# Kernel tuning notes

Measured on AMD Instinct MI355X. Metric: run time of the kernel, lower is better.

## Reference

```python
import jax, jax.numpy as jnp
import numpy as np

B, NQ, NK, DIM, H = 2, 2048, 4096, 256, 8
HD = DIM // H  # head dim = 32


def setup_inputs() -> dict:
    key = jax.random.key(0)
    ks = jax.random.split(key, 8)
    s = 0.02  # init scale for weights
    return {
        "xq": jax.random.normal(ks[0], (B, NQ, DIM), jnp.float32),
        "xk": jax.random.normal(ks[1], (B, NK, DIM), jnp.float32),
        "xv": jax.random.normal(ks[2], (B, NK, DIM), jnp.float32),
        # torch nn.Linear weights: shape (out, in), y = x @ W.T + b
        "wq": jax.random.normal(ks[3], (DIM, DIM), jnp.float32) * s,
        "wk": jax.random.normal(ks[4], (DIM, DIM), jnp.float32) * s,
        "wv": jax.random.normal(ks[5], (DIM, DIM), jnp.float32) * s,
        "wp": jax.random.normal(ks[6], (DIM, DIM), jnp.float32) * s,
        "bp": jnp.zeros((DIM,), jnp.float32),
    }


def reference(xq, xk, xv, wq, wk, wv, wp, bp):
    scale = HD ** (-0.5)
    Bq, Nq, C = xq.shape
    Nk = xk.shape[1]
    # project and split heads: [B, H, N, HD]
    q = jnp.einsum('bnc,dc->bnd', xq, wq).reshape(Bq, Nq, H, HD).transpose(0, 2, 1, 3)
    k = jnp.einsum('bnc,dc->bnd', xk, wk).reshape(Bq, Nk, H, HD).transpose(0, 2, 1, 3)
    v = jnp.einsum('bnc,dc->bnd', xv, wv).reshape(Bq, Nk, H, HD).transpose(0, 2, 1, 3)
    # pre-softmax scores [B, H, Nq, Nk]
    attn = jnp.einsum('bhqd,bhkd->bhqk', q, k) * scale
    attn_save = attn.sum(axis=1) / H  # head-mean of pre-softmax scores
    p = jax.nn.softmax(attn, axis=-1)
    x = jnp.einsum('bhqk,bhkd->bhqd', p, v).transpose(0, 2, 1, 3).reshape(Bq, Nq, C)
    x = jnp.einsum('bnc,dc->bnd', x, wp) + bp
    return x, attn_save
```

## Files before the change

### kernel.cpp

```cpp
#include <hip/hip_runtime.h>

typedef unsigned int u32;
typedef unsigned short u16;
typedef short bf16x8 __attribute__((ext_vector_type(8)));
typedef float f32x4 __attribute__((ext_vector_type(4)));
typedef int i32x4 __attribute__((ext_vector_type(4)));
typedef __bf16 bf16x2 __attribute__((ext_vector_type(2)));
typedef float f32x2 __attribute__((ext_vector_type(2)));

#define KSPLIT 4

__device__ __forceinline__ u32 pack2bf(float a, float b) {
    u32 ua = __float_as_uint(a), ub = __float_as_uint(b);
    ua = (ua + 0x7fffu + ((ua >> 16) & 1u)) >> 16;
    ub = (ub + 0x7fffu + ((ub >> 16) & 1u)) >> 16;
    return (ua & 0xffffu) | (ub << 16);
}
__device__ __forceinline__ u16 bf1(float a) {
    u32 ua = __float_as_uint(a);
    return (u16)((ua + 0x7fffu + ((ua >> 16) & 1u)) >> 16);
}
__device__ __forceinline__ u32 b2(float a, float b) {
    f32x2 f; f[0] = a; f[1] = b;
    bf16x2 h = __builtin_convertvector(f, bf16x2);
    return __builtin_bit_cast(u32, h);
}

__global__ __launch_bounds__(256) void cvt_w4(const float* __restrict__ wq,
                                              const float* __restrict__ wk,
                                              const float* __restrict__ wv,
                                              const float* __restrict__ wp,
                                              u16* __restrict__ dst) {
    int i = blockIdx.x * 256 + threadIdx.x;
    int which = i >> 14;
    int j = i & 16383;
    const float* s = which == 0 ? wq : which == 1 ? wk : which == 2 ? wv : wp;
    float4 a = ((const float4*)s)[j];
    uint2 v;
    v.x = pack2bf(a.x, a.y);
    v.y = pack2bf(a.z, a.w);
    ((uint2*)(dst + which * 65536))[j] = v;
}

__global__ __launch_bounds__(256) void proj_all(const float* __restrict__ xq,
                                                const float* __restrict__ xk,
                                                const float* __restrict__ xv,
                                                const u16* __restrict__ W4,
                                                u16* __restrict__ Qb,
                                                u16* __restrict__ K2,
                                                u16* __restrict__ V2,
                                                float qalpha) {
    int bx = blockIdx.x;
    int mode = bx < 64 ? 0 : (bx < 192 ? 1 : 2);
    int xb = mode == 0 ? bx : (mode == 1 ? bx - 64 : bx - 192);
    const float* X = mode == 0 ? xq : mode == 1 ? xk : xv;
    const u16* Wb = W4 + mode * 65536;

    __shared__ u16 xs[64 * 256];
    int t = threadIdx.x;
    int m0 = xb * 64;
#pragma unroll
    for (int i = 0; i < 8; i++) {
        int c16 = t + 256 * i;
        int row = c16 >> 5, col16 = c16 & 31;
        const float4* src = (const float4*)(X + (size_t)(m0 + row) * 256 + col16 * 8);
        float4 a = src[0], b2v = src[1];
        uint4 v;
        v.x = pack2bf(a.x, a.y); v.y = pack2bf(a.z, a.w);
        v.z = pack2bf(b2v.x, b2v.y); v.w = pack2bf(b2v.z, b2v.w);
        int byteoff = row * 512 + ((col16 * 16) ^ ((row & 7) << 4));
        *(uint4*)((char*)xs + byteoff) = v;
    }
    __syncthreads();
    int lane = t & 63, w = t >> 6;
    int lq = lane & 15, g = lane >> 4;
    int rowA = w * 16 + lq;
    f32x4 acc[16];
    f32x4 z = {0.f, 0.f, 0.f, 0.f};
#pragma unroll
    for (int nt = 0; nt < 16; nt++) acc[nt] = z;
#pragma unroll
    for (int kk = 0; kk < 8; kk++) {
        bf16x8 aF = *(const bf16x8*)((const char*)xs + rowA * 512 +
                                     ((kk * 64 + g * 16) ^ ((rowA & 7) << 4)));
#pragma unroll
        for (int nt = 0; nt < 16; nt++) {
            bf16x8 bF = *(const bf16x8*)(Wb + (size_t)(nt * 16 + lq) * 256 + kk * 32 + g * 8);
            acc[nt] = __builtin_amdgcn_mfma_f32_16x16x32_bf16(aF, bF, acc[nt], 0, 0, 0);
        }
    }
    if (mode == 0) {
#pragma unroll
        for (int nt = 0; nt < 16; nt++) {
            int col = nt * 16 + lq;
#pragma unroll
            for (int r = 0; r < 4; r++) {
                int m = m0 + w * 16 + g * 4 + r;
                Qb[(size_t)m * 256 + col] = bf1(acc[nt][r] * qalpha);
            }
        }
    } else if (mode == 1) {
        int m = m0 + w * 16 + g * 4;
        int b = m >> 12, n = m & 4095;
#pragma unroll
        for (int nt = 0; nt < 16; nt++) {
            int d = nt * 16 + lq;
            int h = d >> 5, d32 = d & 31;
            u16* p = K2 + ((size_t)(b * 8 + h) * 4096 + n) * 32 + d32;
#pragma unroll
            for (int r = 0; r < 4; r++) p[r * 32] = bf1(acc[nt][r]);
        }
    } else {
        int m = m0 + w * 16 + g * 4;
        int b = m >> 12, n = m & 4095;
        int s = n >> 5, rem = n & 31;
        int hp = rem >> 4, gp = (rem >> 2) & 3;
        int pklo = gp * 8 + hp * 4;
#pragma unroll
        for (int nt = 0; nt < 16; nt++) {
            int d = nt * 16 + lq;
            int h = d >> 5, d32 = d & 31;
            uint2 v;
            v.x = pack2bf(acc[nt][0], acc[nt][1]);
            v.y = pack2bf(acc[nt][2], acc[nt][3]);
            *(uint2*)(V2 + ((((size_t)(b * 8 + h) * 128 + s) * 32 + d32) * 32 + pklo)) = v;
        }
    }
}

__global__ __launch_bounds__(256) void save_gemm(const u16* __restrict__ Qb,
                                                 const u16* __restrict__ K2,
                                                 float* __restrict__ sv) {
    const float SAVE = 0.125f * 0.69314718055994530942f;
    int b = blockIdx.z;
    int m0 = blockIdx.y * 128, n0 = blockIdx.x * 128;
    int t = threadIdx.x, lane = t & 63, wv = t >> 6;
    int wr = wv >> 1, wc = wv & 1;
    int lq = lane & 15, g = lane >> 4;
    const u16* Q = Qb + (size_t)b * 2048 * 256;
    f32x4 acc[4][4];
    f32x4 z = {0.f, 0.f, 0.f, 0.f};
#pragma unroll
    for (int mt = 0; mt < 4; mt++)
#pragma unroll
        for (int nt = 0; nt < 4; nt++) acc[mt][nt] = z;
#pragma unroll
    for (int kk = 0; kk < 8; kk++) {
        bf16x8 aF[4], bF[4];
#pragma unroll
        for (int mt = 0; mt < 4; mt++)
            aF[mt] = *(const bf16x8*)(Q + (size_t)(m0 + wr * 64 + mt * 16 + lq) * 256 + kk * 32 + g * 8);
#pragma unroll
        for (int nt = 0; nt < 4; nt++)
            bF[nt] = *(const bf16x8*)(K2 + ((size_t)(b * 8 + kk) * 4096 + n0 + wc * 64 + nt * 16 + lq) * 32 + g * 8);
#pragma unroll
        for (int mt = 0; mt < 4; mt++)
#pragma unroll
            for (int nt = 0; nt < 4; nt++)
                acc[mt][nt] = __builtin_amdgcn_mfma_f32_16x16x32_bf16(aF[mt], bF[nt], acc[mt][nt], 0, 0, 0);
    }
#pragma unroll
    for (int mt = 0; mt < 4; mt++) {
#pragma unroll
        for (int nt = 0; nt < 4; nt++) {
            int col = n0 + wc * 64 + nt * 16 + lq;
#pragma unroll
            for (int r = 0; r < 4; r++) {
                int row = m0 + wr * 64 + mt * 16 + g * 4 + r;
                sv[((size_t)b * 2048 + row) * 4096 + col] = acc[mt][nt][r] * SAVE;
            }
        }
    }
}

__global__ __launch_bounds__(256, 4) void attn_part(const u16* __restrict__ Qb,
                                                    const u16* __restrict__ K2,
                                                    const u16* __restrict__ V2,
                                                    float* __restrict__ PO,
                                                    float* __restrict__ PL) {
    int b = blockIdx.z >> 2, part = blockIdx.z & 3, h = blockIdx.y;
    int bh = b * 8 + h;
    int t = threadIdx.x, lane = t & 63, w = t >> 6;
    int lq = lane & 15, g = lane >> 4;
    int qa = blockIdx.x * 128 + w * 32 + lq;
    const u16* Qrow = Qb + ((size_t)(b * 2048 + qa)) * 256 + h * 32 + g * 8;
    bf16x8 qFa = *(const bf16x8*)Qrow;
    bf16x8 qFb = *(const bf16x8*)(Qrow + 16 * 256);
    const u16* Kh = K2 + ((size_t)bh * 4096 + part * 1024 + lq) * 32 + g * 8;
    const u16* Vh = V2 + ((size_t)bh * 128 + part * 32) * 1024 + lq * 32 + g * 8;
    f32x4 z4 = {0.f, 0.f, 0.f, 0.f};
    f32x4 oa0 = z4, oa1 = z4, ob0 = z4, ob1 = z4, laa = z4, lab = z4;
    const short ONE = (short)0x3F80;
    bf16x8 onesF = {ONE, ONE, ONE, ONE, ONE, ONE, ONE, ONE};
    for (int it = 0; it < 16; ++it) {
        const u16* kp = Kh + it * 2048;
        bf16x8 kF0 = *(const bf16x8*)(kp);
        bf16x8 kF1 = *(const bf16x8*)(kp + 512);
        bf16x8 kF2 = *(const bf16x8*)(kp + 1024);
        bf16x8 kF3 = *(const bf16x8*)(kp + 1536);
        f32x4 sa[4], sb[4];
        sa[0] = __builtin_amdgcn_mfma_f32_16x16x32_bf16(kF0, qFa, z4, 0, 0, 0);
        sa[1] = __builtin_amdgcn_mfma_f32_16x16x32_bf16(kF1, qFa, z4, 0, 0, 0);
        sa[2] = __builtin_amdgcn_mfma_f32_16x16x32_bf16(kF2, qFa, z4, 0, 0, 0);
        sa[3] = __builtin_amdgcn_mfma_f32_16x16x32_bf16(kF3, qFa, z4, 0, 0, 0);
        sb[0] = __builtin_amdgcn_mfma_f32_16x16x32_bf16(kF0, qFb, z4, 0, 0, 0);
        sb[1] = __builtin_amdgcn_mfma_f32_16x16x32_bf16(kF1, qFb, z4, 0, 0, 0);
        sb[2] = __builtin_amdgcn_mfma_f32_16x16x32_bf16(kF2, qFb, z4, 0, 0, 0);
        sb[3] = __builtin_amdgcn_mfma_f32_16x16x32_bf16(kF3, qFb, z4, 0, 0, 0);
        u32 ua[8], ub[8];
#pragma unroll
        for (int kt = 0; kt < 4; kt++) {
            float a0 = __builtin_amdgcn_exp2f(sa[kt][0]);
            float a1 = __builtin_amdgcn_exp2f(sa[kt][1]);
            float a2 = __builtin_amdgcn_exp2f(sa[kt][2]);
            float a3 = __builtin_amdgcn_exp2f(sa[kt][3]);
            ua[2 * kt] = b2(a0, a1);
            ua[2 * kt + 1] = b2(a2, a3);
            float b0 = __builtin_amdgcn_exp2f(sb[kt][0]);
            float b1 = __builtin_amdgcn_exp2f(sb[kt][1]);
            float b2v = __builtin_amdgcn_exp2f(sb[kt][2]);
            float b3 = __builtin_amdgcn_exp2f(sb[kt][3]);
            ub[2 * kt] = b2(b0, b1);
            ub[2 * kt + 1] = b2(b2v, b3);
        }
#pragma unroll
        for (int s = 0; s < 2; s++) {
            const u16* vp = Vh + (it * 2 + s) * 1024;
            bf16x8 vF0 = *(const bf16x8*)(vp);
            bf16x8 vF1 = *(const bf16x8*)(vp + 512);
            i32x4 wa, wb;
            wa[0] = (int)ua[4 * s]; wa[1] = (int)ua[4 * s + 1];
            wa[2] = (int)ua[4 * s + 2]; wa[3] = (int)ua[4 * s + 3];
            wb[0] = (int)ub[4 * s]; wb[1] = (int)ub[4 * s + 1];
            wb[2] = (int)ub[4 * s + 2]; wb[3] = (int)ub[4 * s + 3];
            bf16x8 pa = __builtin_bit_cast(bf16x8, wa);
            bf16x8 pb = __builtin_bit_cast(bf16x8, wb);
            laa = __builtin_amdgcn_mfma_f32_16x16x32_bf16(onesF, pa, laa, 0, 0, 0);
            lab = __builtin_amdgcn_mfma_f32_16x16x32_bf16(onesF, pb, lab, 0, 0, 0);
            oa0 = __builtin_amdgcn_mfma_f32_16x16x32_bf16(vF0, pa, oa0, 0, 0, 0);
            oa1 = __builtin_amdgcn_mfma_f32_16x16x32_bf16(vF1, pa, oa1, 0, 0, 0);
            ob0 = __builtin_amdgcn_mfma_f32_16x16x32_bf16(vF0, pb, ob0, 0, 0, 0);
            ob1 = __builtin_amdgcn_mfma_f32_16x16x32_bf16(vF1, pb, ob1, 0, 0, 0);
        }
    }
    size_t rowa = (size_t)(part * 16 + bh) * 2048 + qa;
    float* poa = PO + rowa * 32;
    *(f32x4*)(poa + g * 4) = oa0;
    *(f32x4*)(poa + 16 + g * 4) = oa1;
    float* pob = PO + (rowa + 16) * 32;
    *(f32x4*)(pob + g * 4) = ob0;
    *(f32x4*)(pob + 16 + g * 4) = ob1;
    if (g == 0) {
        PL[rowa] = laa[0];
        PL[rowa + 16] = lab[0];
    }
}

__global__ __launch_bounds__(256) void attn_combine(const float* __restrict__ PO,
                                                    const float* __restrict__ PL,
                                                    u16* __restrict__ Ob) {
    int idx = blockIdx.x * 256 + threadIdx.x;
    int bh = idx >> 11, q = idx & 2047;
    f32x4 acc[8];
    f32x4 z = {0.f, 0.f, 0.f, 0.f};
#pragma unroll
    for (int j = 0; j < 8; j++) acc[j] = z;
    float L = 0.f;
#pragma unroll
    for (int p = 0; p < KSPLIT; p++) {
        int i = ((p * 16 + bh) << 11) + q;
        L += PL[i];
        const f32x4* src = (const f32x4*)(PO + ((size_t)i * 32));
#pragma unroll
        for (int j = 0; j < 8; j++) acc[j] += src[j];
    }
    float inv = 1.0f / L;
    u16* dst = Ob + ((size_t)((bh >> 3) * 2048 + q)) * 256 + (bh & 7) * 32;
    u32 words[16];
#pragma unroll
    for (int j = 0; j < 8; j++) {
        words[2 * j] = pack2bf(acc[j][0] * inv, acc[j][1] * inv);
        words[2 * j + 1] = pack2bf(acc[j][2] * inv, acc[j][3] * inv);
    }
#pragma unroll
    for (int v = 0; v < 4; v++) {
        uint4 t4;
        t4.x = words[4 * v]; t4.y = words[4 * v + 1]; t4.z = words[4 * v + 2]; t4.w = words[4 * v + 3];
        *(uint4*)(dst + v * 8) = t4;
    }
}

__global__ __launch_bounds__(64) void oproj(const u16* __restrict__ Ob,
                                            const u16* __restrict__ Wp,
                                            const float* __restrict__ bp,
                                            float* __restrict__ out) {
    int t = threadIdx.x, lq = t & 15, g = t >> 4;
    int m0 = blockIdx.x * 16;
    int nb = blockIdx.y * 4;
    f32x4 acc[4];
    f32x4 z = {0.f, 0.f, 0.f, 0.f};
#pragma unroll
    for (int j = 0; j < 4; j++) acc[j] = z;
#pragma unroll
    for (int kk = 0; kk < 8; kk++) {
        bf16x8 aF = *(const bf16x8*)(Ob + (size_t)(m0 + lq) * 256 + kk * 32 + g * 8);
#pragma unroll
        for (int j = 0; j < 4; j++) {
            bf16x8 bF = *(const bf16x8*)(Wp + (size_t)((nb + j) * 16 + lq) * 256 + kk * 32 + g * 8);
            acc[j] = __builtin_amdgcn_mfma_f32_16x16x32_bf16(aF, bF, acc[j], 0, 0, 0);
        }
    }
#pragma unroll
    for (int j = 0; j < 4; j++) {
        int col = (nb + j) * 16 + lq;
        float bias = bp[col];
#pragma unroll
        for (int r = 0; r < 4; r++) {
            int row = m0 + g * 4 + r;
            out[(size_t)row * 256 + col] = acc[j][r] + bias;
        }
    }
}

extern "C" void kernel_launch(void* const* d_in, const int* in_sizes, int n_in,
                              void* d_out, int out_size, void* d_ws, size_t ws_size,
                              hipStream_t stream) {
    const float* xq = (const float*)d_in[0];
    const float* xk = (const float*)d_in[1];
    const float* xv = (const float*)d_in[2];
    const float* wq = (const float*)d_in[3];
    const float* wk = (const float*)d_in[4];
    const float* wv = (const float*)d_in[5];
    const float* wp = (const float*)d_in[6];
    const float* bp = (const float*)d_in[7];
    float* out = (float*)d_out;

    u16* wsb = (u16*)d_ws;
    u16* W4 = wsb;
    u16* WPb = wsb + 196608;
    u16* Qb = wsb + 262144;
    u16* K2 = Qb + 1048576;
    u16* V2 = K2 + 2097152;
    u16* Ob = V2 + 2097152;

    float* outw = out + 1048576;
    float* PO = outw;
    float* PL = PO + 4194304;

    const float qalpha = 0.17677669529663687f * 1.4426950408889634f;

    cvt_w4<<<256, 256, 0, stream>>>(wq, wk, wv, wp, W4);
    proj_all<<<320, 256, 0, stream>>>(xq, xk, xv, W4, Qb, K2, V2, qalpha);

    attn_part<<<dim3(16, 8, 2 * KSPLIT), 256, 0, stream>>>(Qb, K2, V2, PO, PL);
    attn_combine<<<128, 256, 0, stream>>>(PO, PL, Ob);
    oproj<<<dim3(256, 4), 64, 0, stream>>>(Ob, WPb, bp, out);

    save_gemm<<<dim3(32, 16, 2), 256, 0, stream>>>(Qb, K2, out + 1048576);
}
```

Baseline: 126.1 us.

## Switch attention kernel to 32x32x16 MFMA tiles with scalar row-sum

Rewrites the split-K attention kernel to use 32x32x16 bf16 MFMA instead of 16x16x32. Each wave now handles 64 queries and the softmax denominator is summed in registers plus a lane shuffle, replacing the ones-vector MFMA. The V layout permutation in the projection kernel changes to match the new operand layout. The grid is flattened to 1D with heads innermost to improve K/V cache sharing, and launch bounds drop to 2 blocks per SIMD to allow more registers, which reduces occupancy.

Result: faster. 116.7 us (-7.4%).

```diff
diff --git a/kernel.cpp b/kernel.cpp
--- a/kernel.cpp
+++ b/kernel.cpp
@@ -4,6 +4,7 @@
 typedef unsigned short u16;
 typedef short bf16x8 __attribute__((ext_vector_type(8)));
 typedef float f32x4 __attribute__((ext_vector_type(4)));
+typedef float f32x16 __attribute__((ext_vector_type(16)));
 typedef int i32x4 __attribute__((ext_vector_type(4)));
 typedef __bf16 bf16x2 __attribute__((ext_vector_type(2)));
 typedef float f32x2 __attribute__((ext_vector_type(2)));
@@ -113,9 +114,9 @@
     } else {
         int m = m0 + w * 16 + g * 4;
         int b = m >> 12, n = m & 4095;
-        int s = n >> 5, rem = n & 31;
-        int hp = rem >> 4, gp = (rem >> 2) & 3;
-        int pklo = gp * 8 + hp * 4;
+        int s = n >> 5;
+        int t5 = n & 31;
+        int pklo = (t5 & 19) | ((t5 << 1) & 8) | ((t5 >> 1) & 4);
 #pragma unroll
         for (int nt = 0; nt < 16; nt++) {
             int d = nt * 16 + lq;
@@ -173,86 +174,87 @@
     }
 }
 
-__global__ __launch_bounds__(256, 4) void attn_part(const u16* __restrict__ Qb,
+__global__ __launch_bounds__(256, 2) void attn_part(const u16* __restrict__ Qb,
                                                     const u16* __restrict__ K2,
                                                     const u16* __restrict__ V2,
                                                     float* __restrict__ PO,
                                                     float* __restrict__ PL) {
-    int b = blockIdx.z >> 2, part = blockIdx.z & 3, h = blockIdx.y;
+    int id = blockIdx.x;
+    int h = id & 7;
+    int r0 = id >> 3;
+    int qblk = r0 & 7;
+    int b = (r0 >> 3) & 1;
+    int part = r0 >> 4;
     int bh = b * 8 + h;
     int t = threadIdx.x, lane = t & 63, w = t >> 6;
-    int lq = lane & 15, g = lane >> 4;
-    int qa = blockIdx.x * 128 + w * 32 + lq;
-    const u16* Qrow = Qb + ((size_t)(b * 2048 + qa)) * 256 + h * 32 + g * 8;
-    bf16x8 qFa = *(const bf16x8*)Qrow;
-    bf16x8 qFb = *(const bf16x8*)(Qrow + 16 * 256);
-    const u16* Kh = K2 + ((size_t)bh * 4096 + part * 1024 + lq) * 32 + g * 8;
-    const u16* Vh = V2 + ((size_t)bh * 128 + part * 32) * 1024 + lq * 32 + g * 8;
-    f32x4 z4 = {0.f, 0.f, 0.f, 0.f};
-    f32x4 oa0 = z4, oa1 = z4, ob0 = z4, ob1 = z4, laa = z4, lab = z4;
-    const short ONE = (short)0x3F80;
-    bf16x8 onesF = {ONE, ONE, ONE, ONE, ONE, ONE, ONE, ONE};
+    int lq = lane & 31, hl = lane >> 5;
+    int qa = qblk * 256 + w * 64 + lq;
+    const u16* Qrow = Qb + ((size_t)(b * 2048 + qa)) * 256 + h * 32 + hl * 8;
+    bf16x8 qf00 = *(const bf16x8*)(Qrow);
+    bf16x8 qf01 = *(const bf16x8*)(Qrow + 16);
+    bf16x8 qf10 = *(const bf16x8*)(Qrow + 32 * 256);
+    bf16x8 qf11 = *(const bf16x8*)(Qrow + 32 * 256 + 16);
+    const u16* Kh = K2 + ((size_t)bh * 4096 + part * 1024 + lq) * 32 + hl * 8;
+    const u16* Vh = V2 + (size_t)bh * 131072 + part * 32768 + lq * 32 + hl * 8;
+    f32x16 z16 = {};
+    f32x16 o0 = z16, o1 = z16;
+    float l0 = 0.f, l1 = 0.f;
     for (int it = 0; it < 16; ++it) {
-        const u16* kp = Kh + it * 2048;
-        bf16x8 kF0 = *(const bf16x8*)(kp);
-        bf16x8 kF1 = *(const bf16x8*)(kp + 512);
-        bf16x8 kF2 = *(const bf16x8*)(kp + 1024);
-        bf16x8 kF3 = *(const bf16x8*)(kp + 1536);
-        f32x4 sa[4], sb[4];
-        sa[0] = __builtin_amdgcn_mfma_f32_16x16x32_bf16(kF0, qFa, z4, 0, 0, 0);
-        sa[1] = __builtin_amdgcn_mfma_f32_16x16x32_bf16(kF1, qFa, z4, 0, 0, 0);
-        sa[2] = __builtin_amdgcn_mfma_f32_16x16x32_bf16(kF2, qFa, z4, 0, 0, 0);
-        sa[3] = __builtin_amdgcn_mfma_f32_16x16x32_bf16(kF3, qFa, z4, 0, 0, 0);
-        sb[0] = __builtin_amdgcn_mfma_f32_16x16x32_bf16(kF0, qFb, z4, 0, 0, 0);
-        sb[1] = __builtin_amdgcn_mfma_f32_16x16x32_bf16(kF1, qFb, z4, 0, 0, 0);
-        sb[2] = __builtin_amdgcn_mfma_f32_16x16x32_bf16(kF2, qFb, z4, 0, 0, 0);
-        sb[3] = __builtin_amdgcn_mfma_f32_16x16x32_bf16(kF3, qFb, z4, 0, 0, 0);
-        u32 ua[8], ub[8];
-#pragma unroll
-        for (int kt = 0; kt < 4; kt++) {
-            float a0 = __builtin_amdgcn_exp2f(sa[kt][0]);
-            float a1 = __builtin_amdgcn_exp2f(sa[kt][1]);
-            float a2 = __builtin_amdgcn_exp2f(sa[kt][2]);
-            float a3 = __builtin_amdgcn_exp2f(sa[kt][3]);
-            ua[2 * kt] = b2(a0, a1);
-            ua[2 * kt + 1] = b2(a2, a3);
-            float b0 = __builtin_amdgcn_exp2f(sb[kt][0]);
-            float b1 = __builtin_amdgcn_exp2f(sb[kt][1]);
-            float b2v = __builtin_amdgcn_exp2f(sb[kt][2]);
-            float b3 = __builtin_amdgcn_exp2f(sb[kt][3]);
-            ub[2 * kt] = b2(b0, b1);
-            ub[2 * kt + 1] = b2(b2v, b3);
-        }
 #pragma unroll
         for (int s = 0; s < 2; s++) {
+            const u16* kp = Kh + (it * 64 + s * 32) * 32;
+            bf16x8 kf0 = *(const bf16x8*)(kp);
+            bf16x8 kf1 = *(const bf16x8*)(kp + 16);
             const u16* vp = Vh + (it * 2 + s) * 1024;
-            bf16x8 vF0 = *(const bf16x8*)(vp);
-            bf16x8 vF1 = *(const bf16x8*)(vp + 512);
-            i32x4 wa, wb;
-            wa[0] = (int)ua[4 * s]; wa[1] = (int)ua[4 * s + 1];
-            wa[2] = (int)ua[4 * s + 2]; wa[3] = (int)ua[4 * s + 3];
-            wb[0] = (int)ub[4 * s]; wb[1] = (int)ub[4 * s + 1];
-            wb[2] = (int)ub[4 * s + 2]; wb[3] = (int)ub[4 * s + 3];
-            bf16x8 pa = __builtin_bit_cast(bf16x8, wa);
-            bf16x8 pb = __builtin_bit_cast(bf16x8, wb);
-            laa = __builtin_amdgcn_mfma_f32_16x16x32_bf16(onesF, pa, laa, 0, 0, 0);
-            lab = __builtin_amdgcn_mfma_f32_16x16x32_bf16(onesF, pb, lab, 0, 0, 0);
-            oa0 = __builtin_amdgcn_mfma_f32_16x16x32_bf16(vF0, pa, oa0, 0, 0, 0);
-            oa1 = __builtin_amdgcn_mfma_f32_16x16x32_bf16(vF1, pa, oa1, 0, 0, 0);
-            ob0 = __builtin_amdgcn_mfma_f32_16x16x32_bf16(vF0, pb, ob0, 0, 0, 0);
-            ob1 = __builtin_amdgcn_mfma_f32_16x16x32_bf16(vF1, pb, ob1, 0, 0, 0);
-        }
-    }
+            bf16x8 vf0 = *(const bf16x8*)(vp);
+            bf16x8 vf1 = *(const bf16x8*)(vp + 16);
+            f32x16 sA = __builtin_amdgcn_mfma_f32_32x32x16_bf16(kf0, qf00, z16, 0, 0, 0);
+            sA = __builtin_amdgcn_mfma_f32_32x32x16_bf16(kf1, qf01, sA, 0, 0, 0);
+            f32x16 sB = __builtin_amdgcn_mfma_f32_32x32x16_bf16(kf0, qf10, z16, 0, 0, 0);
+            sB = __builtin_amdgcn_mfma_f32_32x32x16_bf16(kf1, qf11, sB, 0, 0, 0);
+            float pA[16], pB[16];
+#pragma unroll
+            for (int k = 0; k < 16; k++) pA[k] = __builtin_amdgcn_exp2f(sA[k]);
+#pragma unroll
+            for (int k = 0; k < 16; k++) pB[k] = __builtin_amdgcn_exp2f(sB[k]);
+            float la = 0.f, lb = 0.f;
+#pragma unroll
+            for (int k = 0; k < 16; k++) { la += pA[k]; lb += pB[k]; }
+            l0 += la; l1 += lb;
+            i32x4 wa0, wa1, wb0, wb1;
+#pragma unroll
+            for (int j = 0; j < 4; j++) {
+                wa0[j] = (int)b2(pA[2 * j], pA[2 * j + 1]);
+                wa1[j] = (int)b2(pA[8 + 2 * j], pA[9 + 2 * j]);
+                wb0[j] = (int)b2(pB[2 * j], pB[2 * j + 1]);
+                wb1[j] = (int)b2(pB[8 + 2 * j], pB[9 + 2 * j]);
+            }
+            bf16x8 pa0 = __builtin_bit_cast(bf16x8, wa0);
+            bf16x8 pa1 = __builtin_bit_cast(bf16x8, wa1);
+            bf16x8 pb0 = __builtin_bit_cast(bf16x8, wb0);
+            bf16x8 pb1 = __builtin_bit_cast(bf16x8, wb1);
+            o0 = __builtin_amdgcn_mfma_f32_32x32x16_bf16(vf0, pa0, o0, 0, 0, 0);
+            o0 = __builtin_amdgcn_mfma_f32_32x32x16_bf16(vf1, pa1, o0, 0, 0, 0);
+            o1 = __builtin_amdgcn_mfma_f32_32x32x16_bf16(vf0, pb0, o1, 0, 0, 0);
+            o1 = __builtin_amdgcn_mfma_f32_32x32x16_bf16(vf1, pb1, o1, 0, 0, 0);
+        }
+    }
+    l0 += __shfl_xor(l0, 32);
+    l1 += __shfl_xor(l1, 32);
     size_t rowa = (size_t)(part * 16 + bh) * 2048 + qa;
     float* poa = PO + rowa * 32;
-    *(f32x4*)(poa + g * 4) = oa0;
-    *(f32x4*)(poa + 16 + g * 4) = oa1;
-    float* pob = PO + (rowa + 16) * 32;
-    *(f32x4*)(pob + g * 4) = ob0;
-    *(f32x4*)(pob + 16 + g * 4) = ob1;
-    if (g == 0) {
-        PL[rowa] = laa[0];
-        PL[rowa + 16] = lab[0];
+    float* pob = PO + (rowa + 32) * 32;
+#pragma unroll
+    for (int cc = 0; cc < 4; cc++) {
+        f32x4 va, vb;
+#pragma unroll
+        for (int i = 0; i < 4; i++) { va[i] = o0[4 * cc + i]; vb[i] = o1[4 * cc + i]; }
+        *(f32x4*)(poa + cc * 8 + hl * 4) = va;
+        *(f32x4*)(pob + cc * 8 + hl * 4) = vb;
+    }
+    if (hl == 0) {
+        PL[rowa] = l0;
+        PL[rowa + 32] = l1;
     }
 }
 
@@ -352,7 +354,7 @@
     cvt_w4<<<256, 256, 0, stream>>>(wq, wk, wv, wp, W4);
     proj_all<<<320, 256, 0, stream>>>(xq, xk, xv, W4, Qb, K2, V2, qalpha);
 
-    attn_part<<<dim3(16, 8, 2 * KSPLIT), 256, 0, stream>>>(Qb, K2, V2, PO, PL);
+    attn_part<<<512, 256, 0, stream>>>(Qb, K2, V2, PO, PL);
     attn_combine<<<128, 256, 0, stream>>>(PO, PL, Ob);
     oproj<<<dim3(256, 4), 64, 0, stream>>>(Ob, WPb, bp, out);
 
```
